# Kernel tuning notes

Hardware: AMD Instinct MI355X
Metric: run time of the kernel (lower is better)

The kernel has to match this reference:

```python
import jax, jax.numpy as jnp
import numpy as np

B, H, N, D, K2 = 4, 8, 4096, 64, 16  # batch, heads, seq_len, dim, k//2


def setup_inputs() -> dict:
    key = jax.random.key(0)
    k1, k2, k3, k4 = jax.random.split(key, 4)
    x = jax.random.normal(k1, (B, H, N, D), dtype=jnp.float32)
    decay = jax.random.uniform(k2, (1, 2 * N, 1), dtype=jnp.float32)
    cos = jax.random.uniform(k3, (1, 2 * N, K2, 1), dtype=jnp.float32) * 2.0 - 1.0
    coef = jax.random.normal(k4, (H, 1, K2, D), dtype=jnp.float32)
    index = jnp.arange(N, dtype=jnp.int32)
    return {"x": x, "decay": decay, "cos": cos, "coef": coef, "index": index}


def reference(x, decay, cos, coef, index):
    n = x.shape[-2]
    # a: (h, 2n, d) implicit long-conv filter from low-rank cosine basis + decay
    a = decay * jnp.sum(coef * cos, axis=-2)
    a = a[None]  # (1, h, 2n, d) to match x's rank
    y = jnp.fft.rfft(x, 2 * n, axis=-2)      # (b, h, 2n//2+1, d) complex
    v = jnp.fft.rfft(a, 2 * n, axis=-2)      # (1, h, 2n//2+1, d) complex
    out = jnp.fft.irfft(v * y, 2 * n, axis=-2)  # circular conv of length 2n
    return jnp.take(out, index, axis=-2)     # keep first n positions
```

## Files before the change

kernel.cpp:

```cpp
#include <hip/hip_runtime.h>
#include <math.h>

#define NB 4
#define NH 8
#define NN 4096
#define ND 64
#define NK 16
#define MM 8192
#define LOG2M 13
#define NT 512

__device__ __forceinline__ void fft_dif(float2* A, int tid) {
    for (int s = LOG2M - 1; s >= 0; --s) {
        __syncthreads();
        const int half = 1 << s;
        const float cmul = -(float)M_PI / (float)half;
        #pragma unroll 1
        for (int b = tid; b < MM / 2; b += NT) {
            int pos = b & (half - 1);
            int i0  = ((b >> s) << (s + 1)) + pos;
            int i1  = i0 + half;
            float2 u = A[i0];
            float2 v = A[i1];
            float sn, cs;
            __sincosf(cmul * (float)pos, &sn, &cs);
            float2 t = make_float2(u.x - v.x, u.y - v.y);
            A[i0] = make_float2(u.x + v.x, u.y + v.y);
            A[i1] = make_float2(t.x * cs - t.y * sn, t.x * sn + t.y * cs);
        }
    }
    __syncthreads();
}

__device__ __forceinline__ void fft_dit_inv(float2* A, int tid) {
    for (int s = 0; s < LOG2M; ++s) {
        __syncthreads();
        const int half = 1 << s;
        const float cmul = (float)M_PI / (float)half;
        #pragma unroll 1
        for (int b = tid; b < MM / 2; b += NT) {
            int pos = b & (half - 1);
            int i0  = ((b >> s) << (s + 1)) + pos;
            int i1  = i0 + half;
            float2 u = A[i0];
            float2 v = A[i1];
            float sn, cs;
            __sincosf(cmul * (float)pos, &sn, &cs);
            float2 t = make_float2(v.x * cs - v.y * sn, v.x * sn + v.y * cs);
            A[i1] = make_float2(u.x - t.x, u.y - t.y);
            A[i0] = make_float2(u.x + t.x, u.y + t.y);
        }
    }
    __syncthreads();
}

__global__ __launch_bounds__(NT, 1)
void fftconv_kernel(const float* __restrict__ x,
                    const float* __restrict__ decay,
                    const float* __restrict__ cosb,
                    const float* __restrict__ coef,
                    float* __restrict__ out)
{
    __shared__ float2 V[MM];
    __shared__ float2 X[MM];

    int bid = blockIdx.x;
    int wg  = (bid & 7) * 64 + (bid >> 3);
    int h   = wg >> 6;
    int d   = wg & 63;
    int tid = threadIdx.x;

    float cf[NK];
    #pragma unroll
    for (int k = 0; k < NK; ++k)
        cf[k] = coef[(h * NK + k) * ND + d];

    for (int u = tid; u < MM; u += NT) {
        const float4* cr = (const float4*)(cosb + (size_t)u * NK);
        float4 c0 = cr[0], c1 = cr[1], c2 = cr[2], c3 = cr[3];
        float acc = c0.x*cf[0]  + c0.y*cf[1]  + c0.z*cf[2]  + c0.w*cf[3]
                  + c1.x*cf[4]  + c1.y*cf[5]  + c1.z*cf[6]  + c1.w*cf[7]
                  + c2.x*cf[8]  + c2.y*cf[9]  + c2.z*cf[10] + c2.w*cf[11]
                  + c3.x*cf[12] + c3.y*cf[13] + c3.z*cf[14] + c3.w*cf[15];
        V[u] = make_float2(decay[u] * acc, 0.0f);
    }

    fft_dif(V, tid);

    const float inv_m = 1.0f / (float)MM;
    for (int bp = 0; bp < 2; ++bp) {
        const int b0 = 2 * bp, b1 = 2 * bp + 1;
        const float* x0 = x + ((size_t)(b0 * NH + h) * NN) * ND + d;
        const float* x1 = x + ((size_t)(b1 * NH + h) * NN) * ND + d;

        __syncthreads();
        for (int u = tid; u < NN; u += NT)
            X[u] = make_float2(x0[(size_t)u * ND], x1[(size_t)u * ND]);
        for (int u = NN + tid; u < MM; u += NT)
            X[u] = make_float2(0.0f, 0.0f);

        fft_dif(X, tid);

        for (int u = tid; u < MM; u += NT) {
            float2 a_ = X[u], f_ = V[u];
            X[u] = make_float2(a_.x * f_.x - a_.y * f_.y,
                               a_.x * f_.y + a_.y * f_.x);
        }

        fft_dit_inv(X, tid);

        float* o0 = out + ((size_t)(b0 * NH + h) * NN) * ND + d;
        float* o1 = out + ((size_t)(b1 * NH + h) * NN) * ND + d;
        for (int u = tid; u < NN; u += NT) {
            float2 z = X[u];
            o0[(size_t)u * ND] = z.x * inv_m;
            o1[(size_t)u * ND] = z.y * inv_m;
        }
    }
}

extern "C" void kernel_launch(void* const* d_in, const int* in_sizes, int n_in,
                              void* d_out, int out_size, void* d_ws, size_t ws_size,
                              hipStream_t stream) {
    const float* x     = (const float*)d_in[0];
    const float* decay = (const float*)d_in[1];
    const float* cosb  = (const float*)d_in[2];
    const float* coef  = (const float*)d_in[3];
    float* out = (float*)d_out;

    hipLaunchKernelGGL(fftconv_kernel, dim3(NH * ND), dim3(NT), 0, stream,
                       x, decay, cosb, coef, out);
}
```

Baseline: 268.1 us.

## Replace radix-2 shared-memory FFT with register radix-16 passes and swizzled LDS

Replaces the 13-stage radix-2 shared-memory FFT, which synchronises after every stage, with three radix-16 passes done in registers. Shared memory is used only for transposes between passes, with an XOR swizzle to avoid bank conflicts. The filter spectrum stays in registers, so one shared buffer replaces two and more blocks can share a CU (launch bounds 4). The last radix-2 stage is fused into the pointwise multiply. Costs are higher register pressure and twiddle factors built by repeated squaring, which may lose some precision.

Result: slower. 488.3 us (+82.1%).

```diff
diff --git a/kernel.cpp b/kernel.cpp
--- a/kernel.cpp
+++ b/kernel.cpp
@@ -7,114 +7,237 @@
 #define ND 64
 #define NK 16
 #define MM 8192
-#define LOG2M 13
 #define NT 512
 
-__device__ __forceinline__ void fft_dif(float2* A, int tid) {
-    for (int s = LOG2M - 1; s >= 0; --s) {
-        __syncthreads();
-        const int half = 1 << s;
-        const float cmul = -(float)M_PI / (float)half;
-        #pragma unroll 1
-        for (int b = tid; b < MM / 2; b += NT) {
-            int pos = b & (half - 1);
-            int i0  = ((b >> s) << (s + 1)) + pos;
-            int i1  = i0 + half;
-            float2 u = A[i0];
-            float2 v = A[i1];
-            float sn, cs;
-            __sincosf(cmul * (float)pos, &sn, &cs);
-            float2 t = make_float2(u.x - v.x, u.y - v.y);
-            A[i0] = make_float2(u.x + v.x, u.y + v.y);
-            A[i1] = make_float2(t.x * cs - t.y * sn, t.x * sn + t.y * cs);
-        }
-    }
+__device__ __forceinline__ int swz(int i) { return i ^ (((i >> 5) & 15) << 1); }
+
+__device__ __forceinline__ float2 cadd(float2 a, float2 b){ return make_float2(a.x+b.x, a.y+b.y); }
+__device__ __forceinline__ float2 csub(float2 a, float2 b){ return make_float2(a.x-b.x, a.y-b.y); }
+__device__ __forceinline__ float2 cmul(float2 a, float2 b){ return make_float2(a.x*b.x-a.y*b.y, a.x*b.y+a.y*b.x); }
+
+template<int B, bool INV>
+__device__ __forceinline__ void fft_regs(float2 r[16], int t)
+{
+    const int lo = t & ((1 << B) - 1);
+    const float S = INV ? 1.0f : -1.0f;
+
+    float2 w3;
+    {
+        float ang = S * (float)M_PI * (float)lo * (1.0f / (float)(1 << (B + 3)));
+        __sincosf(ang, &w3.y, &w3.x);
+    }
+    const float2 w2 = cmul(w3, w3);
+    const float2 w1 = cmul(w2, w2);
+    const float2 w0 = cmul(w1, w1);
+
+    const float c8 = 0.92387953251128674f;
+    const float s8 = 0.38268343236508978f;
+    const float rh = 0.70710678118654752f;
+    const float C3x[8] = {1.f, c8, rh, s8, 0.f, -s8, -rh, -c8};
+    const float C3y[8] = {0.f, s8, rh, c8, 1.f,  c8,  rh,  s8};
+
+#define BF_F(i0, i1, W) { float2 u_=r[i0], v_=r[i1]; r[i0]=cadd(u_,v_); r[i1]=cmul(csub(u_,v_), (W)); }
+#define BF_I(i0, i1, W) { float2 t_=cmul(r[i1], (W)); float2 u_=r[i0]; r[i0]=cadd(u_,t_); r[i1]=csub(u_,t_); }
+
+    if (!INV) {
+        #pragma unroll
+        for (int k = 0; k < 8; ++k) {
+            float2 W = cmul(w3, make_float2(C3x[k], S*C3y[k]));
+            BF_F(k, k+8, W);
+        }
+        #pragma unroll
+        for (int g = 0; g < 2; ++g)
+        #pragma unroll
+        for (int j = 0; j < 4; ++j) {
+            float2 W = cmul(w2, make_float2(C3x[2*j], S*C3y[2*j]));
+            int k = g*8 + j;
+            BF_F(k, k+4, W);
+        }
+        #pragma unroll
+        for (int g = 0; g < 4; ++g)
+        #pragma unroll
+        for (int j = 0; j < 2; ++j) {
+            float2 W = cmul(w1, make_float2(C3x[4*j], S*C3y[4*j]));
+            int k = g*4 + j;
+            BF_F(k, k+2, W);
+        }
+        #pragma unroll
+        for (int i = 0; i < 8; ++i) {
+            BF_F(2*i, 2*i+1, w0);
+        }
+    } else {
+        #pragma unroll
+        for (int i = 0; i < 8; ++i) {
+            BF_I(2*i, 2*i+1, w0);
+        }
+        #pragma unroll
+        for (int g = 0; g < 4; ++g)
+        #pragma unroll
+        for (int j = 0; j < 2; ++j) {
+            float2 W = cmul(w1, make_float2(C3x[4*j], S*C3y[4*j]));
+            int k = g*4 + j;
+            BF_I(k, k+2, W);
+        }
+        #pragma unroll
+        for (int g = 0; g < 2; ++g)
+        #pragma unroll
+        for (int j = 0; j < 4; ++j) {
+            float2 W = cmul(w2, make_float2(C3x[2*j], S*C3y[2*j]));
+            int k = g*8 + j;
+            BF_I(k, k+4, W);
+        }
+        #pragma unroll
+        for (int k = 0; k < 8; ++k) {
+            float2 W = cmul(w3, make_float2(C3x[k], S*C3y[k]));
+            BF_I(k, k+8, W);
+        }
+    }
+#undef BF_F
+#undef BF_I
+}
+
+__global__ __launch_bounds__(NT, 4)
+void fftconv2_kernel(const float* __restrict__ x,
+                     const float* __restrict__ decay,
+                     const float* __restrict__ cosb,
+                     const float* __restrict__ coef,
+                     float* __restrict__ out)
+{
+    __shared__ float2 Xs[MM];
+
+    const int bid = blockIdx.x;
+    const int wg  = (bid & 7) * 64 + (bid >> 3);
+    const int h   = wg >> 6;
+    const int d   = wg & 63;
+    const int t   = threadIdx.x;
+
+    float2 r[16];
+
+    {
+        float cf[NK];
+        #pragma unroll
+        for (int k = 0; k < NK; ++k) cf[k] = coef[(h * NK + k) * ND + d];
+        #pragma unroll
+        for (int k = 0; k < 16; ++k) {
+            int u = t + k * NT;
+            const float4* cr = (const float4*)(cosb + (size_t)u * NK);
+            float4 c0 = cr[0], c1 = cr[1], c2 = cr[2], c3 = cr[3];
+            float acc = c0.x*cf[0]  + c0.y*cf[1]  + c0.z*cf[2]  + c0.w*cf[3]
+                      + c1.x*cf[4]  + c1.y*cf[5]  + c1.z*cf[6]  + c1.w*cf[7]
+                      + c2.x*cf[8]  + c2.y*cf[9]  + c2.z*cf[10] + c2.w*cf[11]
+                      + c3.x*cf[12] + c3.y*cf[13] + c3.z*cf[14] + c3.w*cf[15];
+            r[k] = make_float2(decay[u] * acc, 0.0f);
+        }
+    }
+    fft_regs<9,false>(r, t);
+    #pragma unroll
+    for (int k = 0; k < 16; ++k) Xs[swz(t + k*NT)] = r[k];
     __syncthreads();
-}
-
-__device__ __forceinline__ void fft_dit_inv(float2* A, int tid) {
-    for (int s = 0; s < LOG2M; ++s) {
-        __syncthreads();
-        const int half = 1 << s;
-        const float cmul = (float)M_PI / (float)half;
-        #pragma unroll 1
-        for (int b = tid; b < MM / 2; b += NT) {
-            int pos = b & (half - 1);
-            int i0  = ((b >> s) << (s + 1)) + pos;
-            int i1  = i0 + half;
-            float2 u = A[i0];
-            float2 v = A[i1];
-            float sn, cs;
-            __sincosf(cmul * (float)pos, &sn, &cs);
-            float2 t = make_float2(v.x * cs - v.y * sn, v.x * sn + v.y * cs);
-            A[i1] = make_float2(u.x - t.x, u.y - t.y);
-            A[i0] = make_float2(u.x + t.x, u.y + t.y);
-        }
+    {
+        const int base5 = (t & 31) + ((t >> 5) << 9);
+        #pragma unroll
+        for (int k = 0; k < 16; ++k) r[k] = Xs[swz(base5 + (k << 5))];
+        fft_regs<5,false>(r, t);
+        #pragma unroll
+        for (int k = 0; k < 16; ++k) Xs[swz(base5 + (k << 5))] = r[k];
     }
     __syncthreads();
-}
-
-__global__ __launch_bounds__(NT, 1)
-void fftconv_kernel(const float* __restrict__ x,
-                    const float* __restrict__ decay,
-                    const float* __restrict__ cosb,
-                    const float* __restrict__ coef,
-                    float* __restrict__ out)
-{
-    __shared__ float2 V[MM];
-    __shared__ float2 X[MM];
-
-    int bid = blockIdx.x;
-    int wg  = (bid & 7) * 64 + (bid >> 3);
-    int h   = wg >> 6;
-    int d   = wg & 63;
-    int tid = threadIdx.x;
-
-    float cf[NK];
+    {
+        const int base1 = (t & 1) + ((t >> 1) << 5);
+        #pragma unroll
+        for (int k = 0; k < 16; ++k) r[k] = Xs[swz(base1 + (k << 1))];
+        fft_regs<1,false>(r, t);
+        #pragma unroll
+        for (int k = 0; k < 16; ++k) Xs[swz(base1 + (k << 1))] = r[k];
+    }
+    __syncthreads();
+    float2 Vr[16];
     #pragma unroll
-    for (int k = 0; k < NK; ++k)
-        cf[k] = coef[(h * NK + k) * ND + d];
-
-    for (int u = tid; u < MM; u += NT) {
-        const float4* cr = (const float4*)(cosb + (size_t)u * NK);
-        float4 c0 = cr[0], c1 = cr[1], c2 = cr[2], c3 = cr[3];
-        float acc = c0.x*cf[0]  + c0.y*cf[1]  + c0.z*cf[2]  + c0.w*cf[3]
-                  + c1.x*cf[4]  + c1.y*cf[5]  + c1.z*cf[6]  + c1.w*cf[7]
-                  + c2.x*cf[8]  + c2.y*cf[9]  + c2.z*cf[10] + c2.w*cf[11]
-                  + c3.x*cf[12] + c3.y*cf[13] + c3.z*cf[14] + c3.w*cf[15];
-        V[u] = make_float2(decay[u] * acc, 0.0f);
-    }
-
-    fft_dif(V, tid);
+    for (int m = 0; m < 8; ++m) {
+        int ph = swz(2 * (t + m * NT));
+        float4 uv = *(const float4*)(&Xs[ph]);
+        float2 u = make_float2(uv.x, uv.y), v = make_float2(uv.z, uv.w);
+        Vr[2*m]   = cadd(u, v);
+        Vr[2*m+1] = csub(u, v);
+    }
 
     const float inv_m = 1.0f / (float)MM;
+    #pragma unroll 1
     for (int bp = 0; bp < 2; ++bp) {
-        const int b0 = 2 * bp, b1 = 2 * bp + 1;
-        const float* x0 = x + ((size_t)(b0 * NH + h) * NN) * ND + d;
-        const float* x1 = x + ((size_t)(b1 * NH + h) * NN) * ND + d;
-
-        __syncthreads();
-        for (int u = tid; u < NN; u += NT)
-            X[u] = make_float2(x0[(size_t)u * ND], x1[(size_t)u * ND]);
-        for (int u = NN + tid; u < MM; u += NT)
-            X[u] = make_float2(0.0f, 0.0f);
-
-        fft_dif(X, tid);
-
-        for (int u = tid; u < MM; u += NT) {
-            float2 a_ = X[u], f_ = V[u];
-            X[u] = make_float2(a_.x * f_.x - a_.y * f_.y,
-                               a_.x * f_.y + a_.y * f_.x);
-        }
-
-        fft_dit_inv(X, tid);
-
-        float* o0 = out + ((size_t)(b0 * NH + h) * NN) * ND + d;
-        float* o1 = out + ((size_t)(b1 * NH + h) * NN) * ND + d;
-        for (int u = tid; u < NN; u += NT) {
-            float2 z = X[u];
-            o0[(size_t)u * ND] = z.x * inv_m;
-            o1[(size_t)u * ND] = z.y * inv_m;
+        const int b0 = 2*bp, b1 = 2*bp + 1;
+        const float* x0 = x + ((size_t)(b0*NH + h) * NN) * ND + d;
+        const float* x1 = x + ((size_t)(b1*NH + h) * NN) * ND + d;
+        __syncthreads();
+
+        #pragma unroll
+        for (int k = 0; k < 8; ++k) {
+            int u = t + k * NT;
+            r[k] = make_float2(x0[(size_t)u * ND], x1[(size_t)u * ND]);
+        }
+        #pragma unroll
+        for (int k = 8; k < 16; ++k) r[k] = make_float2(0.0f, 0.0f);
+        fft_regs<9,false>(r, t);
+        #pragma unroll
+        for (int k = 0; k < 16; ++k) Xs[swz(t + k*NT)] = r[k];
+        __syncthreads();
+        {
+            const int base5 = (t & 31) + ((t >> 5) << 9);
+            #pragma unroll
+            for (int k = 0; k < 16; ++k) r[k] = Xs[swz(base5 + (k << 5))];
+            fft_regs<5,false>(r, t);
+            #pragma unroll
+            for (int k = 0; k < 16; ++k) Xs[swz(base5 + (k << 5))] = r[k];
+        }
+        __syncthreads();
+        {
+            const int base1 = (t & 1) + ((t >> 1) << 5);
+            #pragma unroll
+            for (int k = 0; k < 16; ++k) r[k] = Xs[swz(base1 + (k << 1))];
+            fft_regs<1,false>(r, t);
+            #pragma unroll
+            for (int k = 0; k < 16; ++k) Xs[swz(base1 + (k << 1))] = r[k];
+        }
+        __syncthreads();
+        #pragma unroll
+        for (int m = 0; m < 8; ++m) {
+            int ph = swz(2 * (t + m * NT));
+            float4 uv = *(const float4*)(&Xs[ph]);
+            float2 u = make_float2(uv.x, uv.y), v = make_float2(uv.z, uv.w);
+            float2 y0 = cadd(u, v), y1 = csub(u, v);
+            float2 z0 = cmul(y0, Vr[2*m]);
+            float2 z1 = cmul(y1, Vr[2*m+1]);
+            float2 n0 = cadd(z0, z1), n1 = csub(z0, z1);
+            *(float4*)(&Xs[ph]) = make_float4(n0.x, n0.y, n1.x, n1.y);
+        }
+        __syncthreads();
+        {
+            const int base1 = (t & 1) + ((t >> 1) << 5);
+            #pragma unroll
+            for (int k = 0; k < 16; ++k) r[k] = Xs[swz(base1 + (k << 1))];
+            fft_regs<1,true>(r, t);
+            #pragma unroll
+            for (int k = 0; k < 16; ++k) Xs[swz(base1 + (k << 1))] = r[k];
+        }
+        __syncthreads();
+        {
+            const int base5 = (t & 31) + ((t >> 5) << 9);
+            #pragma unroll
+            for (int k = 0; k < 16; ++k) r[k] = Xs[swz(base5 + (k << 5))];
+            fft_regs<5,true>(r, t);
+            #pragma unroll
+            for (int k = 0; k < 16; ++k) Xs[swz(base5 + (k << 5))] = r[k];
+        }
+        __syncthreads();
+        #pragma unroll
+        for (int k = 0; k < 16; ++k) r[k] = Xs[swz(t + k*NT)];
+        fft_regs<9,true>(r, t);
+        float* o0 = out + ((size_t)(b0*NH + h) * NN) * ND + d;
+        float* o1 = out + ((size_t)(b1*NH + h) * NN) * ND + d;
+        #pragma unroll
+        for (int k = 0; k < 8; ++k) {
+            int u = t + k * NT;
+            o0[(size_t)u * ND] = r[k].x * inv_m;
+            o1[(size_t)u * ND] = r[k].y * inv_m;
         }
     }
 }
@@ -128,6 +251,6 @@
     const float* coef  = (const float*)d_in[3];
     float* out = (float*)d_out;
 
-    hipLaunchKernelGGL(fftconv_kernel, dim3(NH * ND), dim3(NT), 0, stream,
+    hipLaunchKernelGGL(fftconv2_kernel, dim3(NH * ND), dim3(NT), 0, stream,
                        x, decay, cosb, coef, out);
 }
```
